# Performance work log

Measured on AMD Instinct MI355X. Metric: run time of the kernel, lower is better.

## Reference

```python
import jax, jax.numpy as jnp
import numpy as np

VOCAB = 32000
HID = 1024
BATCH = 8
SEQ = 512


def setup_inputs() -> dict:
    key = jax.random.key(0)
    k1, k2, k3, k4 = jax.random.split(key, 4)
    scale = 1.0 / np.sqrt(HID)
    return {
        "batched_sequence_ids": jax.random.randint(k1, (BATCH, SEQ), 0, VOCAB, dtype=jnp.int32),
        "w_out": jax.random.normal(k2, (HID, VOCAB), dtype=jnp.float32) * scale,
        "b_out": jnp.zeros((VOCAB,), dtype=jnp.float32),
        "W_ih": jax.random.normal(k3, (HID, 4 * HID), dtype=jnp.float32) * scale,
        "W_hh": jax.random.normal(k4, (HID, 4 * HID), dtype=jnp.float32) * scale,
        "b_lstm": jnp.zeros((4 * HID,), dtype=jnp.float32),
    }


def _lstm_scan(x_gates, W_hh):
    # x_gates: [B, S, 4H] = precomputed input contribution + bias
    B = x_gates.shape[0]
    H = W_hh.shape[0]
    h0 = jnp.zeros((B, H), dtype=x_gates.dtype)
    c0 = jnp.zeros((B, H), dtype=x_gates.dtype)

    def step(carry, xg_t):
        h, c = carry
        gates = xg_t + h @ W_hh  # [B, 4H]
        i, f, g, o = jnp.split(gates, 4, axis=-1)
        i = jax.nn.sigmoid(i)
        f = jax.nn.sigmoid(f)
        g = jnp.tanh(g)
        o = jax.nn.sigmoid(o)
        c_new = f * c + i * g
        h_new = o * jnp.tanh(c_new)
        return (h_new, c_new), h_new

    # scan over time axis: move S to leading dim
    (_, _), hs = jax.lax.scan(step, (h0, c0), jnp.swapaxes(x_gates, 0, 1))
    return jnp.swapaxes(hs, 0, 1)  # [B, S, H]


def reference(batched_sequence_ids, w_out, b_out, W_ih, W_hh, b_lstm):
    # weight-tied embedding lookup: w_out is [H, V]; emb = w_out[:, ids].T
    emb = jnp.take(w_out.T, batched_sequence_ids, axis=0)  # [B, S, H]
    # precompute input-to-gate contribution for all timesteps in one GEMM
    x_gates = jnp.einsum('bsh,hg->bsg', emb, W_ih) + b_lstm  # [B, S, 4H]
    hs = _lstm_scan(x_gates, W_hh)  # [B, S, H]
    logits = jnp.einsum('bsh,hv->bsv', hs, w_out) + b_out  # [B, S, V]
    return logits
```

## Files before the change

kernel.cpp:

```cpp
#include <hip/hip_runtime.h>
#include <math.h>

#define VOCAB 32000
#define HID   1024
#define BATCH 8
#define SEQ   512
#define GD    (4*HID)
#define ROWS  (BATCH*SEQ)

typedef __attribute__((ext_vector_type(8))) short short8;
typedef __attribute__((ext_vector_type(4))) float f32x4;

__global__ __launch_bounds__(256) void k_gather(const int* __restrict__ ids,
                                                const float* __restrict__ w_out,
                                                float* __restrict__ emb)
{
    int row = blockIdx.x;
    int id  = ids[row];
    const float* src = w_out + id;
    float* dst = emb + (size_t)row * HID;
    for (int h = threadIdx.x; h < HID; h += 256)
        dst[h] = src[(size_t)h * VOCAB];
}

__global__ __launch_bounds__(256) void k_transpose(const float* __restrict__ W,
                                                   float* __restrict__ WT)
{
    __shared__ float tile[32][33];
    int bx = blockIdx.x;
    int by = blockIdx.y;
    int x = bx*32 + threadIdx.x;
    int y = by*32 + threadIdx.y;
    #pragma unroll
    for (int i = 0; i < 32; i += 8)
        tile[threadIdx.y + i][threadIdx.x] = W[(size_t)(y + i)*GD + x];
    __syncthreads();
    int k   = by*32 + threadIdx.x;
    int col = bx*32 + threadIdx.y;
    #pragma unroll
    for (int i = 0; i < 32; i += 8)
        WT[(size_t)(col + i)*HID + k] = tile[threadIdx.x][threadIdx.y + i];
}

#define GBM 128
#define GBN 128
#define GBK 32

__device__ __forceinline__ unsigned pack_hi(float x, float y) {
    return (__float_as_uint(x) >> 16) | (__float_as_uint(y) & 0xFFFF0000u);
}
__device__ __forceinline__ float hi_f32(float x) {
    return __uint_as_float(__float_as_uint(x) & 0xFFFF0000u);
}
__device__ __forceinline__ unsigned pack_pair(float x) {
    unsigned hb = __float_as_uint(x) & 0xFFFF0000u;
    float lo = x - __uint_as_float(hb);
    return hb | (__float_as_uint(lo) >> 16);
}

__global__ __launch_bounds__(256) void k_gemm_mfma(const float* __restrict__ A,
                                                   const float* __restrict__ B,
                                                   const float* __restrict__ bias,
                                                   float* __restrict__ C,
                                                   int M, int N, int K)
{
    __shared__ unsigned short As_hi[GBM][40];
    __shared__ unsigned short As_lo[GBM][40];
    __shared__ unsigned int   Bs[GBK][130];

    int tid  = threadIdx.x;
    int brow = blockIdx.y * GBM;
    int bcol = blockIdx.x * GBN;

    int lane = tid & 63;
    int wid  = tid >> 6;
    int wm   = wid >> 1;
    int wn   = wid & 1;
    int l15  = lane & 15;
    int l4   = lane >> 4;

    int a_m = tid >> 3;
    int a_c = tid & 7;
    int b_k = tid >> 5;
    int b_n = tid & 31;

    f32x4 acc[4][4] = {};

    for (int k0 = 0; k0 < K; k0 += GBK) {
        #pragma unroll
        for (int p = 0; p < 4; ++p) {
            int r = a_m + p*32;
            float4 v = *(const float4*)(A + (size_t)(brow + r)*K + k0 + a_c*4);
            unsigned h0 = pack_hi(v.x, v.y);
            unsigned h1 = pack_hi(v.z, v.w);
            float lx = v.x - hi_f32(v.x);
            float ly = v.y - hi_f32(v.y);
            float lz = v.z - hi_f32(v.z);
            float lw = v.w - hi_f32(v.w);
            unsigned l0 = pack_hi(lx, ly);
            unsigned l1 = pack_hi(lz, lw);
            *(uint2*)&As_hi[r][a_c*4] = make_uint2(h0, h1);
            *(uint2*)&As_lo[r][a_c*4] = make_uint2(l0, l1);
        }
        #pragma unroll
        for (int p = 0; p < 4; ++p) {
            int kk = b_k + p*8;
            float4 v = *(const float4*)(B + (size_t)(k0 + kk)*N + bcol + b_n*4);
            unsigned w0 = pack_pair(v.x);
            unsigned w1 = pack_pair(v.y);
            unsigned w2 = pack_pair(v.z);
            unsigned w3 = pack_pair(v.w);
            *(uint2*)&Bs[kk][b_n*4]     = make_uint2(w0, w1);
            *(uint2*)&Bs[kk][b_n*4 + 2] = make_uint2(w2, w3);
        }
        __syncthreads();

        short8 ah[4], al[4];
        #pragma unroll
        for (int m = 0; m < 4; ++m) {
            int r = wm*64 + m*16 + l15;
            ah[m] = *(const short8*)&As_hi[r][l4*8];
            al[m] = *(const short8*)&As_lo[r][l4*8];
        }

        #pragma unroll
        for (int n = 0; n < 4; ++n) {
            int col = wn*64 + n*16 + l15;
            unsigned w[8];
            #pragma unroll
            for (int j = 0; j < 8; ++j)
                w[j] = Bs[l4*8 + j][col];
            union { short8 v; unsigned d[4]; } bh, bl;
            #pragma unroll
            for (int d = 0; d < 4; ++d) {
                bh.d[d] = (w[2*d] >> 16)      | (w[2*d+1] & 0xFFFF0000u);
                bl.d[d] = (w[2*d] & 0xFFFFu)  | (w[2*d+1] << 16);
            }
            #pragma unroll
            for (int m = 0; m < 4; ++m) {
                acc[m][n] = __builtin_amdgcn_mfma_f32_16x16x32_bf16(ah[m], bh.v, acc[m][n], 0, 0, 0);
                acc[m][n] = __builtin_amdgcn_mfma_f32_16x16x32_bf16(ah[m], bl.v, acc[m][n], 0, 0, 0);
                acc[m][n] = __builtin_amdgcn_mfma_f32_16x16x32_bf16(al[m], bh.v, acc[m][n], 0, 0, 0);
            }
        }
        __syncthreads();
    }

    #pragma unroll
    for (int n = 0; n < 4; ++n) {
        int col = bcol + wn*64 + n*16 + l15;
        float bv = bias[col];
        #pragma unroll
        for (int m = 0; m < 4; ++m) {
            int rb = brow + wm*64 + m*16 + l4*4;
            #pragma unroll
            for (int r = 0; r < 4; ++r)
                C[(size_t)(rb + r)*N + col] = acc[m][n][r] + bv;
        }
    }
}

__global__ __launch_bounds__(256) void k_lstm_step(const float* __restrict__ xg,
                                                   const float* __restrict__ WT,
                                                   float* __restrict__ c_state,
                                                   float* __restrict__ hs,
                                                   int t)
{
    int j    = blockIdx.x;
    int gate = threadIdx.x >> 6;
    int lane = threadIdx.x & 63;
    int col  = gate*HID + j;

    float acc[8] = {};
    if (t > 0) {
        const float4* wv = (const float4*)(WT + (size_t)col*HID);
        #pragma unroll
        for (int c = 0; c < 4; ++c) {
            int k4 = c*64 + lane;
            float4 w4 = wv[k4];
            #pragma unroll
            for (int b = 0; b < 8; ++b) {
                float4 h4 = ((const float4*)(hs + ((size_t)b*SEQ + (t-1))*HID))[k4];
                acc[b] += w4.x*h4.x + w4.y*h4.y + w4.z*h4.z + w4.w*h4.w;
            }
        }
        #pragma unroll
        for (int b = 0; b < 8; ++b) {
            acc[b] += __shfl_xor(acc[b], 32);
            acc[b] += __shfl_xor(acc[b], 16);
            acc[b] += __shfl_xor(acc[b], 8);
            acc[b] += __shfl_xor(acc[b], 4);
            acc[b] += __shfl_xor(acc[b], 2);
            acc[b] += __shfl_xor(acc[b], 1);
        }
    }

    __shared__ float g_sm[4][8];
    if (lane == 0) {
        #pragma unroll
        for (int b = 0; b < 8; ++b)
            g_sm[gate][b] = acc[b];
    }
    __syncthreads();

    if (threadIdx.x < 8) {
        int b = threadIdx.x;
        size_t xbase = ((size_t)b*SEQ + t)*GD + j;
        float iv = g_sm[0][b] + xg[xbase];
        float fv = g_sm[1][b] + xg[xbase + HID];
        float gv = g_sm[2][b] + xg[xbase + 2*HID];
        float ov = g_sm[3][b] + xg[xbase + 3*HID];
        iv = 1.0f / (1.0f + expf(-iv));
        fv = 1.0f / (1.0f + expf(-fv));
        gv = tanhf(gv);
        ov = 1.0f / (1.0f + expf(-ov));
        float c  = (t > 0) ? c_state[(size_t)b*HID + j] : 0.0f;
        float cn = fv*c + iv*gv;
        float hn = ov * tanhf(cn);
        c_state[(size_t)b*HID + j] = cn;
        hs[((size_t)b*SEQ + t)*HID + j] = hn;
    }
}

extern "C" void kernel_launch(void* const* d_in, const int* in_sizes, int n_in,
                              void* d_out, int out_size, void* d_ws, size_t ws_size,
                              hipStream_t stream)
{
    const int*   ids    = (const int*)  d_in[0];
    const float* w_out  = (const float*)d_in[1];
    const float* b_out  = (const float*)d_in[2];
    const float* W_ih   = (const float*)d_in[3];
    const float* W_hh   = (const float*)d_in[4];
    const float* b_lstm = (const float*)d_in[5];
    float* out = (float*)d_out;

    char* ob = (char*)d_out;
    float* emb    = (float*)(ob);
    float* WT     = (float*)(ob + 16777216);
    float* xg     = (float*)(ob + 33554432);
    float* cstate = (float*)(ob + 100663296);
    float* hs     = (float*)d_ws;

    k_gather<<<ROWS, 256, 0, stream>>>(ids, w_out, emb);

    k_transpose<<<dim3(GD/32, HID/32), dim3(32, 8), 0, stream>>>(W_hh, WT);

    k_gemm_mfma<<<dim3(GD/GBN, ROWS/GBM), 256, 0, stream>>>(
        emb, W_ih, b_lstm, xg, ROWS, GD, HID);

    for (int t = 0; t < SEQ; ++t)
        k_lstm_step<<<HID, 256, 0, stream>>>(xg, WT, cstate, hs, t);

    k_gemm_mfma<<<dim3(VOCAB/GBN, ROWS/GBM), 256, 0, stream>>>(
        hs, w_out, b_out, out, ROWS, VOCAB, HID);
}
```

Measured before the change: 5.170 ms.

## Replace per-timestep LSTM launches with persistent kernel and grid barrier

Replaces the 512 per-step LSTM kernel launches with a single persistent kernel of 256 blocks, each owning 4 hidden units. Each block keeps its slice of W_hh in registers across all timesteps and holds the cell state in a register. Steps are separated by an atomic-counter grid barrier with one counter per step. This removes launch overhead and repeated weight reloads, at the cost of relying on all 256 blocks being co-resident and on spin-wait barrier latency.

```diff
diff --git a/kernel.cpp b/kernel.cpp
--- a/kernel.cpp
+++ b/kernel.cpp
@@ -7,6 +7,7 @@
 #define SEQ   512
 #define GD    (4*HID)
 #define ROWS  (BATCH*SEQ)
+#define NBLK  256
 
 typedef __attribute__((ext_vector_type(8))) short short8;
 typedef __attribute__((ext_vector_type(4))) float f32x4;
@@ -160,65 +161,95 @@
     }
 }
 
-__global__ __launch_bounds__(256) void k_lstm_step(const float* __restrict__ xg,
-                                                   const float* __restrict__ WT,
-                                                   float* __restrict__ c_state,
-                                                   float* __restrict__ hs,
-                                                   int t)
-{
-    int j    = blockIdx.x;
-    int gate = threadIdx.x >> 6;
-    int lane = threadIdx.x & 63;
-    int col  = gate*HID + j;
-
-    float acc[8] = {};
-    if (t > 0) {
-        const float4* wv = (const float4*)(WT + (size_t)col*HID);
-        #pragma unroll
-        for (int c = 0; c < 4; ++c) {
-            int k4 = c*64 + lane;
-            float4 w4 = wv[k4];
-            #pragma unroll
-            for (int b = 0; b < 8; ++b) {
-                float4 h4 = ((const float4*)(hs + ((size_t)b*SEQ + (t-1))*HID))[k4];
-                acc[b] += w4.x*h4.x + w4.y*h4.y + w4.z*h4.z + w4.w*h4.w;
-            }
-        }
-        #pragma unroll
-        for (int b = 0; b < 8; ++b) {
-            acc[b] += __shfl_xor(acc[b], 32);
-            acc[b] += __shfl_xor(acc[b], 16);
-            acc[b] += __shfl_xor(acc[b], 8);
-            acc[b] += __shfl_xor(acc[b], 4);
-            acc[b] += __shfl_xor(acc[b], 2);
-            acc[b] += __shfl_xor(acc[b], 1);
-        }
-    }
-
-    __shared__ float g_sm[4][8];
-    if (lane == 0) {
-        #pragma unroll
-        for (int b = 0; b < 8; ++b)
-            g_sm[gate][b] = acc[b];
-    }
-    __syncthreads();
-
-    if (threadIdx.x < 8) {
-        int b = threadIdx.x;
-        size_t xbase = ((size_t)b*SEQ + t)*GD + j;
-        float iv = g_sm[0][b] + xg[xbase];
-        float fv = g_sm[1][b] + xg[xbase + HID];
-        float gv = g_sm[2][b] + xg[xbase + 2*HID];
-        float ov = g_sm[3][b] + xg[xbase + 3*HID];
-        iv = 1.0f / (1.0f + expf(-iv));
-        fv = 1.0f / (1.0f + expf(-fv));
-        gv = tanhf(gv);
-        ov = 1.0f / (1.0f + expf(-ov));
-        float c  = (t > 0) ? c_state[(size_t)b*HID + j] : 0.0f;
-        float cn = fv*c + iv*gv;
-        float hn = ov * tanhf(cn);
-        c_state[(size_t)b*HID + j] = cn;
-        hs[((size_t)b*SEQ + t)*HID + j] = hn;
+__global__ __launch_bounds__(256) void k_lstm_scan(
+    const float* __restrict__ xg, const float* __restrict__ WT,
+    float* __restrict__ hs, unsigned int* __restrict__ bar)
+{
+    const int tid  = threadIdx.x;
+    const int gate = tid >> 6;
+    const int lane = tid & 63;
+    const int j0   = blockIdx.x * 4;
+
+    float4 w[4][4];
+    #pragma unroll
+    for (int jl = 0; jl < 4; ++jl) {
+        const float4* wp = (const float4*)(WT + (size_t)(gate*HID + j0 + jl)*HID);
+        #pragma unroll
+        for (int c = 0; c < 4; ++c)
+            w[jl][c] = wp[c*64 + lane];
+    }
+
+    float creg = 0.0f;
+    __shared__ float g_sm[4][4][8];
+
+    for (int t = 0; t < SEQ; ++t) {
+        float acc[4][8] = {};
+        if (t > 0) {
+            #pragma unroll
+            for (int c = 0; c < 4; ++c) {
+                int k4 = c*64 + lane;
+                #pragma unroll
+                for (int b = 0; b < 8; ++b) {
+                    float4 h4 = ((const float4*)(hs + ((size_t)b*SEQ + (t-1))*HID))[k4];
+                    #pragma unroll
+                    for (int jl = 0; jl < 4; ++jl)
+                        acc[jl][b] += w[jl][c].x*h4.x + w[jl][c].y*h4.y
+                                    + w[jl][c].z*h4.z + w[jl][c].w*h4.w;
+                }
+            }
+            #pragma unroll
+            for (int jl = 0; jl < 4; ++jl)
+                #pragma unroll
+                for (int b = 0; b < 8; ++b) {
+                    float v = acc[jl][b];
+                    v += __shfl_xor(v, 32);
+                    v += __shfl_xor(v, 16);
+                    v += __shfl_xor(v, 8);
+                    v += __shfl_xor(v, 4);
+                    v += __shfl_xor(v, 2);
+                    v += __shfl_xor(v, 1);
+                    acc[jl][b] = v;
+                }
+        }
+        if (lane == 0) {
+            #pragma unroll
+            for (int jl = 0; jl < 4; ++jl)
+                #pragma unroll
+                for (int b = 0; b < 8; ++b)
+                    g_sm[gate][jl][b] = acc[jl][b];
+        }
+        __syncthreads();
+
+        if (tid < 32) {
+            int b  = tid & 7;
+            int jl = tid >> 3;
+            int j  = j0 + jl;
+            size_t xbase = ((size_t)b*SEQ + t)*GD + j;
+            float iv = g_sm[0][jl][b] + xg[xbase];
+            float fv = g_sm[1][jl][b] + xg[xbase + HID];
+            float gv = g_sm[2][jl][b] + xg[xbase + 2*HID];
+            float ov = g_sm[3][jl][b] + xg[xbase + 3*HID];
+            iv = 1.0f / (1.0f + expf(-iv));
+            fv = 1.0f / (1.0f + expf(-fv));
+            gv = tanhf(gv);
+            ov = 1.0f / (1.0f + expf(-ov));
+            float cn = fv*creg + iv*gv;
+            creg = cn;
+            hs[((size_t)b*SEQ + t)*HID + j] = ov * tanhf(cn);
+        }
+
+        if (t < SEQ-1) {
+            __syncthreads();
+            if (tid == 0) {
+                __threadfence();
+                atomicAdd(&bar[t], 1u);
+                while (__hip_atomic_load(&bar[t], __ATOMIC_RELAXED,
+                                         __HIP_MEMORY_SCOPE_AGENT) < NBLK)
+                    __builtin_amdgcn_s_sleep(2);
+            }
+            __syncthreads();
+            __threadfence();
+        }
     }
 }
 
@@ -238,7 +269,7 @@
     float* emb    = (float*)(ob);
     float* WT     = (float*)(ob + 16777216);
     float* xg     = (float*)(ob + 33554432);
-    float* cstate = (float*)(ob + 100663296);
+    unsigned int* bar = (unsigned int*)(ob + 100663296);
     float* hs     = (float*)d_ws;
 
     k_gather<<<ROWS, 256, 0, stream>>>(ids, w_out, emb);
@@ -248,8 +279,8 @@
     k_gemm_mfma<<<dim3(GD/GBN, ROWS/GBM), 256, 0, stream>>>(
         emb, W_ih, b_lstm, xg, ROWS, GD, HID);
 
-    for (int t = 0; t < SEQ; ++t)
-        k_lstm_step<<<HID, 256, 0, stream>>>(xg, WT, cstate, hs, t);
+    hipMemsetAsync((void*)bar, 0, SEQ * sizeof(unsigned int), stream);
+    k_lstm_scan<<<NBLK, 256, 0, stream>>>(xg, WT, hs, bar);
 
     k_gemm_mfma<<<dim3(VOCAB/GBN, ROWS/GBM), 256, 0, stream>>>(
         hs, w_out, b_out, out, ROWS, VOCAB, HID);
```

After: 17.03 ms. 229% more time.

## Pre-split GEMM operands into bf16 hi/lo planes before MFMA GEMMs

Applied to the files above, without the earlier changes.

Adds separate pre-pass kernels that split the A operands into bf16 hi/lo arrays and pack the B weights into hi|lo 32-bit words. A new GEMM kernel loads these pre-converted operands straight into shared memory instead of converting per tile. This removes repeated per-block conversion work, since each B tile is otherwise reconverted by every row-block. The cost is extra passes over the weights and activations, plus extra scratch memory. The output GEMM takes this path only when the workspace is large enough and otherwise falls back to the original kernel.

```diff
diff --git a/kernel.cpp b/kernel.cpp
--- a/kernel.cpp
+++ b/kernel.cpp
@@ -11,16 +11,30 @@
 typedef __attribute__((ext_vector_type(8))) short short8;
 typedef __attribute__((ext_vector_type(4))) float f32x4;
 
-__global__ __launch_bounds__(256) void k_gather(const int* __restrict__ ids,
-                                                const float* __restrict__ w_out,
-                                                float* __restrict__ emb)
+__device__ __forceinline__ float hi_f32(float x) {
+    return __uint_as_float(__float_as_uint(x) & 0xFFFF0000u);
+}
+__device__ __forceinline__ unsigned pack_pair(float x) {
+    unsigned hb = __float_as_uint(x) & 0xFFFF0000u;
+    float lo = x - __uint_as_float(hb);
+    return hb | (__float_as_uint(lo) >> 16);
+}
+
+__global__ __launch_bounds__(256) void k_gather_split(const int* __restrict__ ids,
+                                                      const float* __restrict__ w_out,
+                                                      unsigned short* __restrict__ emb_hi,
+                                                      unsigned short* __restrict__ emb_lo)
 {
     int row = blockIdx.x;
     int id  = ids[row];
     const float* src = w_out + id;
-    float* dst = emb + (size_t)row * HID;
-    for (int h = threadIdx.x; h < HID; h += 256)
-        dst[h] = src[(size_t)h * VOCAB];
+    for (int h = threadIdx.x; h < HID; h += 256) {
+        float v  = src[(size_t)h * VOCAB];
+        float hi = hi_f32(v);
+        float lo = v - hi;
+        emb_hi[(size_t)row*HID + h] = (unsigned short)(__float_as_uint(v)  >> 16);
+        emb_lo[(size_t)row*HID + h] = (unsigned short)(__float_as_uint(lo) >> 16);
+    }
 }
 
 __global__ __launch_bounds__(256) void k_transpose(const float* __restrict__ W,
@@ -42,31 +56,55 @@
         WT[(size_t)(col + i)*HID + k] = tile[threadIdx.x][threadIdx.y + i];
 }
 
+__global__ __launch_bounds__(256) void k_pack_pairs(const float* __restrict__ src,
+                                                    unsigned int* __restrict__ dst,
+                                                    long n4)
+{
+    long i0 = (long)blockIdx.x * 256 + threadIdx.x;
+    long stride = (long)gridDim.x * 256;
+    for (long i = i0; i < n4; i += stride) {
+        float4 v = ((const float4*)src)[i];
+        uint4 o;
+        o.x = pack_pair(v.x); o.y = pack_pair(v.y);
+        o.z = pack_pair(v.z); o.w = pack_pair(v.w);
+        ((uint4*)dst)[i] = o;
+    }
+}
+
+__global__ __launch_bounds__(256) void k_split_f32(const float* __restrict__ src,
+                                                   unsigned short* __restrict__ hi,
+                                                   unsigned short* __restrict__ lo,
+                                                   long n4)
+{
+    long i0 = (long)blockIdx.x * 256 + threadIdx.x;
+    long stride = (long)gridDim.x * 256;
+    for (long i = i0; i < n4; i += stride) {
+        float4 v = ((const float4*)src)[i];
+        unsigned h0 = __float_as_uint(v.x) >> 16, h1 = __float_as_uint(v.y) >> 16;
+        unsigned h2 = __float_as_uint(v.z) >> 16, h3 = __float_as_uint(v.w) >> 16;
+        unsigned l0 = __float_as_uint(v.x - hi_f32(v.x)) >> 16;
+        unsigned l1 = __float_as_uint(v.y - hi_f32(v.y)) >> 16;
+        unsigned l2 = __float_as_uint(v.z - hi_f32(v.z)) >> 16;
+        unsigned l3 = __float_as_uint(v.w - hi_f32(v.w)) >> 16;
+        ((uint2*)hi)[i] = make_uint2(h0 | (h1 << 16), h2 | (h3 << 16));
+        ((uint2*)lo)[i] = make_uint2(l0 | (l1 << 16), l2 | (l3 << 16));
+    }
+}
+
 #define GBM 128
 #define GBN 128
 #define GBK 32
 
-__device__ __forceinline__ unsigned pack_hi(float x, float y) {
-    return (__float_as_uint(x) >> 16) | (__float_as_uint(y) & 0xFFFF0000u);
-}
-__device__ __forceinline__ float hi_f32(float x) {
-    return __uint_as_float(__float_as_uint(x) & 0xFFFF0000u);
-}
-__device__ __forceinline__ unsigned pack_pair(float x) {
-    unsigned hb = __float_as_uint(x) & 0xFFFF0000u;
-    float lo = x - __uint_as_float(hb);
-    return hb | (__float_as_uint(lo) >> 16);
-}
-
-__global__ __launch_bounds__(256) void k_gemm_mfma(const float* __restrict__ A,
-                                                   const float* __restrict__ B,
-                                                   const float* __restrict__ bias,
-                                                   float* __restrict__ C,
-                                                   int M, int N, int K)
+__global__ __launch_bounds__(256) void k_gemm_pre(const unsigned short* __restrict__ Ah,
+                                                  const unsigned short* __restrict__ Al,
+                                                  const unsigned int* __restrict__ Bpk,
+                                                  const float* __restrict__ bias,
+                                                  float* __restrict__ C,
+                                                  int M, int N, int K)
 {
     __shared__ unsigned short As_hi[GBM][40];
     __shared__ unsigned short As_lo[GBM][40];
-    __shared__ unsigned int   Bs[GBK][130];
+    __shared__ unsigned int   Bs[GBK][132];
 
     int tid  = threadIdx.x;
     int brow = blockIdx.y * GBM;
@@ -90,15 +128,109 @@
         #pragma unroll
         for (int p = 0; p < 4; ++p) {
             int r = a_m + p*32;
+            *(uint2*)&As_hi[r][a_c*4] =
+                *(const uint2*)(Ah + (size_t)(brow + r)*K + k0 + a_c*4);
+            *(uint2*)&As_lo[r][a_c*4] =
+                *(const uint2*)(Al + (size_t)(brow + r)*K + k0 + a_c*4);
+        }
+        #pragma unroll
+        for (int p = 0; p < 4; ++p) {
+            int kk = b_k + p*8;
+            *(uint4*)&Bs[kk][b_n*4] =
+                *(const uint4*)(Bpk + (size_t)(k0 + kk)*N + bcol + b_n*4);
+        }
+        __syncthreads();
+
+        short8 ah[4], al[4];
+        #pragma unroll
+        for (int m = 0; m < 4; ++m) {
+            int r = wm*64 + m*16 + l15;
+            ah[m] = *(const short8*)&As_hi[r][l4*8];
+            al[m] = *(const short8*)&As_lo[r][l4*8];
+        }
+
+        #pragma unroll
+        for (int n = 0; n < 4; ++n) {
+            int col = wn*64 + n*16 + l15;
+            unsigned w[8];
+            #pragma unroll
+            for (int j = 0; j < 8; ++j)
+                w[j] = Bs[l4*8 + j][col];
+            union { short8 v; unsigned d[4]; } bh, bl;
+            #pragma unroll
+            for (int d = 0; d < 4; ++d) {
+                bh.d[d] = (w[2*d] >> 16)      | (w[2*d+1] & 0xFFFF0000u);
+                bl.d[d] = (w[2*d] & 0xFFFFu)  | (w[2*d+1] << 16);
+            }
+            #pragma unroll
+            for (int m = 0; m < 4; ++m) {
+                acc[m][n] = __builtin_amdgcn_mfma_f32_16x16x32_bf16(ah[m], bh.v, acc[m][n], 0, 0, 0);
+                acc[m][n] = __builtin_amdgcn_mfma_f32_16x16x32_bf16(ah[m], bl.v, acc[m][n], 0, 0, 0);
+                acc[m][n] = __builtin_amdgcn_mfma_f32_16x16x32_bf16(al[m], bh.v, acc[m][n], 0, 0, 0);
+            }
+        }
+        __syncthreads();
+    }
+
+    #pragma unroll
+    for (int n = 0; n < 4; ++n) {
+        int col = bcol + wn*64 + n*16 + l15;
+        float bv = bias[col];
+        #pragma unroll
+        for (int m = 0; m < 4; ++m) {
+            int rb = brow + wm*64 + m*16 + l4*4;
+            #pragma unroll
+            for (int r = 0; r < 4; ++r)
+                C[(size_t)(rb + r)*N + col] = acc[m][n][r] + bv;
+        }
+    }
+}
+
+__device__ __forceinline__ unsigned pack_hi2(float x, float y) {
+    return (__float_as_uint(x) >> 16) | (__float_as_uint(y) & 0xFFFF0000u);
+}
+
+__global__ __launch_bounds__(256) void k_gemm_mfma(const float* __restrict__ A,
+                                                   const float* __restrict__ B,
+                                                   const float* __restrict__ bias,
+                                                   float* __restrict__ C,
+                                                   int M, int N, int K)
+{
+    __shared__ unsigned short As_hi[GBM][40];
+    __shared__ unsigned short As_lo[GBM][40];
+    __shared__ unsigned int   Bs[GBK][130];
+
+    int tid  = threadIdx.x;
+    int brow = blockIdx.y * GBM;
+    int bcol = blockIdx.x * GBN;
+
+    int lane = tid & 63;
+    int wid  = tid >> 6;
+    int wm   = wid >> 1;
+    int wn   = wid & 1;
+    int l15  = lane & 15;
+    int l4   = lane >> 4;
+
+    int a_m = tid >> 3;
+    int a_c = tid & 7;
+    int b_k = tid >> 5;
+    int b_n = tid & 31;
+
+    f32x4 acc[4][4] = {};
+
+    for (int k0 = 0; k0 < K; k0 += GBK) {
+        #pragma unroll
+        for (int p = 0; p < 4; ++p) {
+            int r = a_m + p*32;
             float4 v = *(const float4*)(A + (size_t)(brow + r)*K + k0 + a_c*4);
-            unsigned h0 = pack_hi(v.x, v.y);
-            unsigned h1 = pack_hi(v.z, v.w);
+            unsigned h0 = pack_hi2(v.x, v.y);
+            unsigned h1 = pack_hi2(v.z, v.w);
             float lx = v.x - hi_f32(v.x);
             float ly = v.y - hi_f32(v.y);
             float lz = v.z - hi_f32(v.z);
             float lw = v.w - hi_f32(v.w);
-            unsigned l0 = pack_hi(lx, ly);
-            unsigned l1 = pack_hi(lz, lw);
+            unsigned l0 = pack_hi2(lx, ly);
+            unsigned l1 = pack_hi2(lz, lw);
             *(uint2*)&As_hi[r][a_c*4] = make_uint2(h0, h1);
             *(uint2*)&As_lo[r][a_c*4] = make_uint2(l0, l1);
         }
@@ -235,22 +367,40 @@
     float* out = (float*)d_out;
 
     char* ob = (char*)d_out;
-    float* emb    = (float*)(ob);
-    float* WT     = (float*)(ob + 16777216);
-    float* xg     = (float*)(ob + 33554432);
-    float* cstate = (float*)(ob + 100663296);
-    float* hs     = (float*)d_ws;
-
-    k_gather<<<ROWS, 256, 0, stream>>>(ids, w_out, emb);
+    unsigned short* emb_hi = (unsigned short*)(ob);
+    unsigned short* emb_lo = (unsigned short*)(ob + 8388608);
+    float*          WT     = (float*)(ob + 16777216);
+    float*          xg     = (float*)(ob + 33554432);
+    float*          cstate = (float*)(ob + 100663296);
+    unsigned int*   wih_pk = (unsigned int*)(ob + 100696064);
+
+    char* wb = (char*)d_ws;
+    float* hs = (float*)wb;
+    const size_t NEED = 16777216ull + 8388608ull*2 + (size_t)VOCAB*HID*4ull;
+    const bool big_ws = (ws_size >= NEED);
+    unsigned short* hs_hi = (unsigned short*)(wb + 16777216);
+    unsigned short* hs_lo = (unsigned short*)(wb + 25165824);
+    unsigned int*   wo_pk = (unsigned int*)(wb + 33554432);
+
+    k_gather_split<<<ROWS, 256, 0, stream>>>(ids, w_out, emb_hi, emb_lo);
 
     k_transpose<<<dim3(GD/32, HID/32), dim3(32, 8), 0, stream>>>(W_hh, WT);
 
-    k_gemm_mfma<<<dim3(GD/GBN, ROWS/GBM), 256, 0, stream>>>(
-        emb, W_ih, b_lstm, xg, ROWS, GD, HID);
+    k_pack_pairs<<<1024, 256, 0, stream>>>(W_ih, wih_pk, (long)HID*GD/4);
+
+    k_gemm_pre<<<dim3(GD/GBN, ROWS/GBM), 256, 0, stream>>>(
+        emb_hi, emb_lo, wih_pk, b_lstm, xg, ROWS, GD, HID);
 
     for (int t = 0; t < SEQ; ++t)
         k_lstm_step<<<HID, 256, 0, stream>>>(xg, WT, cstate, hs, t);
 
-    k_gemm_mfma<<<dim3(VOCAB/GBN, ROWS/GBM), 256, 0, stream>>>(
-        hs, w_out, b_out, out, ROWS, VOCAB, HID);
-}
+    if (big_ws) {
+        k_pack_pairs<<<2048, 256, 0, stream>>>(w_out, wo_pk, (long)HID*VOCAB/4);
+        k_split_f32<<<1024, 256, 0, stream>>>(hs, hs_hi, hs_lo, (long)ROWS*HID/4);
+        k_gemm_pre<<<dim3(VOCAB/GBN, ROWS/GBM), 256, 0, stream>>>(
+            hs_hi, hs_lo, wo_pk, b_out, out, ROWS, VOCAB, HID);
+    } else {
+        k_gemm_mfma<<<dim3(VOCAB/GBN, ROWS/GBM), 256, 0, stream>>>(
+            hs, w_out, b_out, out, ROWS, VOCAB, HID);
+    }
+}
```

After: 5.313 ms. 2.8% more time.
